# Performance work log

Measured on AMD Instinct MI355X. Metric: run time of the kernel, lower is better.

Reference implementation:

```python
import jax, jax.numpy as jnp
from jax import lax
import numpy as np

B, T = 32, 64
E, H, V = 512, 512, 10000


def setup_inputs() -> dict:
    key = jax.random.key(0)
    ks = jax.random.split(key, 9)
    s = 0.02
    return {
        "features": jax.random.normal(ks[0], (B, E), dtype=jnp.float32),
        "captions": jax.random.randint(ks[1], (B, T), 0, V, dtype=jnp.int64),
        "forward_approach": 0,
        "embed_table": jax.random.normal(ks[2], (V, E), dtype=jnp.float32) * s,
        "W_ih": jax.random.normal(ks[3], (4 * H, E), dtype=jnp.float32) * s,
        "W_hh": jax.random.normal(ks[4], (4 * H, H), dtype=jnp.float32) * s,
        "b_ih": jax.random.normal(ks[5], (4 * H,), dtype=jnp.float32) * s,
        "b_hh": jax.random.normal(ks[6], (4 * H,), dtype=jnp.float32) * s,
        "fc_W": jax.random.normal(ks[7], (V, H), dtype=jnp.float32) * s,
        "fc_b": jax.random.normal(ks[8], (V,), dtype=jnp.float32) * s,
    }


def reference(features, captions, forward_approach, embed_table,
              W_ih, W_hh, b_ih, b_hh, fc_W, fc_b):
    # features: [B, E]; captions: [B, T] int
    batch = features.shape[0]
    seq_len = captions.shape[1]
    hidden = W_hh.shape[1]

    # Input at step 0 is `features`; at step t>0 it is embed(captions[:, t-1]).
    emb = embed_table[captions[:, : seq_len - 1]]            # [B, T-1, E]
    xs = jnp.concatenate([features[None], jnp.transpose(emb, (1, 0, 2))],
                         axis=0)                              # [T, B, E]

    def step(carry, x):
        h, c = carry
        # PyTorch LSTMCell gate order: i, f, g, o
        gates = x @ W_ih.T + b_ih + h @ W_hh.T + b_hh         # [B, 4H]
        i, f, g, o = jnp.split(gates, 4, axis=-1)
        i = jax.nn.sigmoid(i)
        f = jax.nn.sigmoid(f)
        g = jnp.tanh(g)
        o = jax.nn.sigmoid(o)
        c = f * c + i * g
        h = o * jnp.tanh(c)
        return (h, c), h

    h0 = jnp.zeros((batch, hidden), dtype=features.dtype)
    c0 = jnp.zeros((batch, hidden), dtype=features.dtype)
    _, hs = lax.scan(step, (h0, c0), xs)                      # [T, B, H]

    logits = jnp.einsum('tbh,vh->tbv', hs, fc_W) + fc_b       # [T, B, V]
    return jnp.transpose(logits, (1, 0, 2))                   # [B, T, V]
```

## Files before the change

### kernel.cpp

```cpp
#include <hip/hip_runtime.h>
#include <hip/hip_bf16.h>

#define B_ 32
#define T_ 64
#define E_ 512
#define H_ 512
#define V_ 10000
#define G4 2048

#define NLSTM 64
#define NFC   157
#define NTOT  (NLSTM + NFC)

using bf16x8 = __attribute__((ext_vector_type(8))) short;
using f32x4  = __attribute__((ext_vector_type(4))) float;

__device__ inline f32x4 mfma16(bf16x8 a, bf16x8 b, f32x4 c) {
  return __builtin_amdgcn_mfma_f32_16x16x32_bf16(a, b, c, 0, 0, 0);
}

__device__ inline short f2bf(float x) {
  unsigned u = __builtin_bit_cast(unsigned, x);
  u = (u + 0x7fffu + ((u >> 16) & 1u)) >> 16;
  return (short)u;
}

__device__ inline float fsigm(float x) {
  return __builtin_amdgcn_rcpf(1.f + __builtin_amdgcn_exp2f(-1.442695040888963f * x));
}
__device__ inline float ftanh(float x) {
  return 1.f - 2.f * __builtin_amdgcn_rcpf(1.f + __builtin_amdgcn_exp2f(2.885390081777927f * x));
}

__device__ inline bf16x8 lds_ld16B(const short* base, int row, int col) {
  int byte = (row << 10) + (col << 1);
  byte ^= (row & 7) << 4;
  return *(const bf16x8*)((const char*)base + byte);
}

__device__ inline bf16x8 cast8(const float* src) {
  float4 f0 = *(const float4*)src;
  float4 f1 = *(const float4*)(src + 4);
  bf16x8 v;
  v[0] = f2bf(f0.x); v[1] = f2bf(f0.y); v[2] = f2bf(f0.z); v[3] = f2bf(f0.w);
  v[4] = f2bf(f1.x); v[5] = f2bf(f1.y); v[6] = f2bf(f1.z); v[7] = f2bf(f1.w);
  return v;
}


__global__ void prep_kernel(const float* __restrict__ b_ih, const float* __restrict__ b_hh,
                            const float* __restrict__ features, const int* __restrict__ captions,
                            const float* __restrict__ embed,
                            float* __restrict__ bsum, short* __restrict__ xs) {
  int i = blockIdx.x * blockDim.x + threadIdx.x;
  int stride = gridDim.x * blockDim.x;
  const int NA = G4;
  const int NB = NA + T_ * B_ * E_;
  for (; i < NB; i += stride) {
    if (i < NA) {
      bsum[i] = b_ih[i] + b_hh[i];
    } else {
      int j = i - NA;
      int t = j / (B_ * E_);
      int r = j - t * (B_ * E_);
      int b = r >> 9;
      int e = r & 511;
      float v;
      if (t == 0) v = features[b * E_ + e];
      else        v = embed[captions[b * T_ + (t - 1)] * E_ + e];
      xs[j] = f2bf(v);
    }
  }
}


__global__ __launch_bounds__(256) void fused_kernel(const float* __restrict__ WhhF,
                                                    const float* __restrict__ WihF,
                                                    const float* __restrict__ bsum,
                                                    const short* __restrict__ xs,
                                                    short* __restrict__ hs,
                                                    int* __restrict__ flags,
                                                    const float* __restrict__ fcWF,
                                                    const float* __restrict__ fcbias,
                                                    float* __restrict__ out) {
  __shared__ short Wlds[2 * 64 * 512];
  __shared__ int tready;
  const int tid = threadIdx.x;
  int* const cnt = flags + 256;

  if (blockIdx.x < NLSTM) {
    const int blk  = blockIdx.x;
    const int bg   = blk >> 5;
    const int slot = blk & 31;
    const int hc0  = slot * 16;
    int* const gflags = flags + bg * 32;

    for (int i = tid * 8; i < 2 * 64 * 512; i += 256 * 8) {
      int region = i >> 15;
      int local  = i & 32767;
      int gc = local >> 9;
      int k  = local & 511;
      int g  = gc >> 4, c = gc & 15;
      const float* src = (region ? WihF : WhhF) + (size_t)(g * 512 + hc0 + c) * 512 + k;
      bf16x8 v = cast8(src);
      int byte = ((local * 2) ^ ((gc & 7) << 4)) + (region << 16);
      *(bf16x8*)((char*)Wlds + byte) = v;
    }
    __syncthreads();
    if (tid >= 64) return;

    const short* WB = Wlds + 64 * 512;
    const int lane = tid;
    const int lr  = lane & 15;
    const int ko  = (lane >> 4) << 3;
    const int cr  = (lane >> 4) << 2;
    const int cc  = lane & 15;
    const int bat = bg * 16 + cc;
    const int brow = bg * 16 + lr;

    float4 bb0 = *(const float4*)&bsum[0 * 512 + hc0 + cr];
    float4 bb1 = *(const float4*)&bsum[1 * 512 + hc0 + cr];
    float4 bb2 = *(const float4*)&bsum[2 * 512 + hc0 + cr];
    float4 bb3 = *(const float4*)&bsum[3 * 512 + hc0 + cr];

    float cst[4] = {0.f, 0.f, 0.f, 0.f};

    for (int t = 0; t < T_; ++t) {
      f32x4 a0 = {}, a1 = {}, a2 = {}, a3 = {};
      {
        const short* Ax = xs + ((size_t)t * B_ + brow) * 512 + ko;
#pragma unroll
        for (int kk = 0; kk < 512; kk += 32) {
          bf16x8 xb = *(const bf16x8*)(Ax + kk);
          bf16x8 w0 = lds_ld16B(WB,      lr, kk + ko);
          bf16x8 w1 = lds_ld16B(WB, 16 + lr, kk + ko);
          bf16x8 w2 = lds_ld16B(WB, 32 + lr, kk + ko);
          bf16x8 w3 = lds_ld16B(WB, 48 + lr, kk + ko);
          a0 = mfma16(w0, xb, a0);
          a1 = mfma16(w1, xb, a1);
          a2 = mfma16(w2, xb, a2);
          a3 = mfma16(w3, xb, a3);
        }
      }
      if (t > 0) {
        const int* fp = gflags + (lane & 31);
        for (;;) {
          int fl = __hip_atomic_load(fp, __ATOMIC_RELAXED, __HIP_MEMORY_SCOPE_AGENT);
          if (__all(fl >= t)) break;
        }
        asm volatile("" ::: "memory");
        const short* Ap = hs + (size_t)(t - 1) * (B_ * H_) + brow * 512 + ko;
#pragma unroll
        for (int kk = 0; kk < 512; kk += 32) {
          bf16x8 hb = *(const bf16x8*)(Ap + kk);
          bf16x8 w0 = lds_ld16B(Wlds,      lr, kk + ko);
          bf16x8 w1 = lds_ld16B(Wlds, 16 + lr, kk + ko);
          bf16x8 w2 = lds_ld16B(Wlds, 32 + lr, kk + ko);
          bf16x8 w3 = lds_ld16B(Wlds, 48 + lr, kk + ko);
          a0 = mfma16(w0, hb, a0);
          a1 = mfma16(w1, hb, a1);
          a2 = mfma16(w2, hb, a2);
          a3 = mfma16(w3, hb, a3);
        }
      }
      unsigned long long hpack = 0;
#pragma unroll
      for (int j = 0; j < 4; ++j) {
        float iv = fsigm(a0[j] + ((const float*)&bb0)[j]);
        float fv = fsigm(a1[j] + ((const float*)&bb1)[j]);
        float gv = ftanh(a2[j] + ((const float*)&bb2)[j]);
        float ov = fsigm(a3[j] + ((const float*)&bb3)[j]);
        float cv = fv * cst[j] + iv * gv;
        cst[j] = cv;
        float hv = ov * ftanh(cv);
        hpack |= (unsigned long long)(unsigned short)f2bf(hv) << (16 * j);
      }
      __hip_atomic_store(
          (unsigned long long*)(hs + (size_t)t * (B_ * H_) + bat * 512 + hc0 + cr),
          hpack, __ATOMIC_RELAXED, __HIP_MEMORY_SCOPE_AGENT);
      asm volatile("s_waitcnt vmcnt(0)" ::: "memory");
      if (lane == 0) {
        if (t < T_ - 1)
          __hip_atomic_store(gflags + slot, t + 1, __ATOMIC_RELAXED,
                             __HIP_MEMORY_SCOPE_AGENT);
        __hip_atomic_fetch_add(cnt + t, 1, __ATOMIC_RELAXED,
                               __HIP_MEMORY_SCOPE_AGENT);
      }
    }
  } else {
    const int fblk = blockIdx.x - NLSTM;
    const int n0   = fblk * 64;
    const int lane = tid & 63;
    const int wv   = tid >> 6;
    const int lr   = lane & 15;
    const int ko   = (lane >> 4) << 3;

    if (tid == 0)
      __hip_atomic_store(&tready, 0, __ATOMIC_RELAXED, __HIP_MEMORY_SCOPE_WORKGROUP);

    for (int i = tid * 8; i < 64 * 512; i += 256 * 8) {
      int gc = i >> 9;
      int k  = i & 511;
      int nr = n0 + gc; if (nr >= V_) nr = V_ - 1;
      bf16x8 v = cast8(fcWF + (size_t)nr * 512 + k);
      int byte = (i * 2) ^ ((gc & 7) << 4);
      *(bf16x8*)((char*)Wlds + byte) = v;
    }
    __syncthreads();

    const int cr = (lane >> 4) * 4, cc = lane & 15;
    const int colw = n0 + wv * 16 + cc;
    const bool wok = colw < V_;
    const float bias = wok ? fcbias[colw] : 0.f;

    for (int t = 0; t < T_; ++t) {
      if (wv == 0) {
        for (;;) {
          int c = __hip_atomic_load(cnt + t, __ATOMIC_RELAXED,
                                    __HIP_MEMORY_SCOPE_AGENT);
          if (c >= NLSTM) break;
          __builtin_amdgcn_s_sleep(32);
        }
        __hip_atomic_store(&tready, t + 1, __ATOMIC_RELAXED,
                           __HIP_MEMORY_SCOPE_WORKGROUP);
      } else {
        while (__hip_atomic_load(&tready, __ATOMIC_RELAXED,
                                 __HIP_MEMORY_SCOPE_WORKGROUP) < t + 1)
          __builtin_amdgcn_s_sleep(2);
      }
      asm volatile("" ::: "memory");
      const short* Ap = hs + (size_t)t * (B_ * H_) + lr * 512 + ko;
      f32x4 acc0 = {}, acc1 = {};
#pragma unroll
      for (int k = 0; k < 512; k += 32) {
        bf16x8 a0 = *(const bf16x8*)(Ap + k);
        bf16x8 a1 = *(const bf16x8*)(Ap + 16 * 512 + k);
        bf16x8 b  = lds_ld16B(Wlds, wv * 16 + lr, k + ko);
        acc0 = mfma16(a0, b, acc0);
        acc1 = mfma16(a1, b, acc1);
      }
      if (wok) {
#pragma unroll
        for (int j = 0; j < 4; ++j) {
          out[(size_t)(cr + j) * (T_ * V_) + t * V_ + colw]      = acc0[j] + bias;
          out[(size_t)(16 + cr + j) * (T_ * V_) + t * V_ + colw] = acc1[j] + bias;
        }
      }
    }
  }
}


extern "C" void kernel_launch(void* const* d_in, const int* in_sizes, int n_in,
                              void* d_out, int out_size, void* d_ws, size_t ws_size,
                              hipStream_t stream) {
  const float* features = (const float*)d_in[0];
  const int*   captions = (const int*)d_in[1];
  const float* embed    = (const float*)d_in[3];
  const float* W_ih     = (const float*)d_in[4];
  const float* W_hh     = (const float*)d_in[5];
  const float* b_ih     = (const float*)d_in[6];
  const float* b_hh     = (const float*)d_in[7];
  const float* fc_W     = (const float*)d_in[8];
  const float* fc_b     = (const float*)d_in[9];
  float* out = (float*)d_out;

  char* ws = (char*)d_ws;
  size_t off = 0;
  auto alloc = [&](size_t bytes) -> void* {
    off = (off + 255) & ~(size_t)255;
    void* p = ws + off;
    off += bytes;
    return p;
  };
  int*      flags = (int*)  alloc(4096);
  float*    bsum  = (float*)alloc((size_t)G4 * 4);
  short*    xs    = (short*)alloc((size_t)T_ * B_ * E_ * 2);
  short*    hs    = (short*)alloc((size_t)T_ * B_ * H_ * 2);

  (void)hipMemsetAsync(flags, 0, 4096, stream);
  prep_kernel<<<1024, 256, 0, stream>>>(b_ih, b_hh, features, captions, embed,
                                        bsum, xs);
  fused_kernel<<<NTOT, 256, 0, stream>>>(W_hh, W_ih, bsum, xs, hs, flags,
                                         fc_W, fc_b, out);
}
```

Before: 277.4 us.

## Map LSTM groups to single XCDs and sync recurrence via XCD-local flags

```diff
diff --git a/kernel.cpp b/kernel.cpp
--- a/kernel.cpp
+++ b/kernel.cpp
@@ -8,9 +8,8 @@
 #define V_ 10000
 #define G4 2048
 
-#define NLSTM 64
 #define NFC   157
-#define NTOT  (NLSTM + NFC)
+#define NTOT  256
 
 using bf16x8 = __attribute__((ext_vector_type(8))) short;
 using f32x4  = __attribute__((ext_vector_type(4))) float;
@@ -79,116 +78,201 @@
                                                     const float* __restrict__ bsum,
                                                     const short* __restrict__ xs,
                                                     short* __restrict__ hs,
-                                                    int* __restrict__ flags,
+                                                    int* __restrict__ comm,
                                                     const float* __restrict__ fcWF,
                                                     const float* __restrict__ fcbias,
                                                     float* __restrict__ out) {
   __shared__ short Wlds[2 * 64 * 512];
   __shared__ int tready;
+  __shared__ int hmail;
   const int tid = threadIdx.x;
-  int* const cnt = flags + 256;
-
-  if (blockIdx.x < NLSTM) {
-    const int blk  = blockIdx.x;
-    const int bg   = blk >> 5;
-    const int slot = blk & 31;
+  const int m8  = blockIdx.x & 7;
+  int* const cnt = comm + 256;
+
+  if (m8 < 2) {
+    const int g    = m8;
+    const int slot = blockIdx.x >> 3;
     const int hc0  = slot * 16;
-    int* const gflags = flags + bg * 32;
-
+    int* const gflags = comm + g * 32;
+    int* const lflags = comm + 64 + g * 32;
+    int* const pub    = comm + 128 + g * 32;
+
+    unsigned xcd;
+    asm volatile("s_getreg_b32 %0, hwreg(HW_REG_XCC_ID)" : "=s"(xcd));
+    if (tid == 0) {
+      tready = 0;
+      hmail  = 0;
+      __hip_atomic_store(pub + slot, (int)(xcd & 7) + 1, __ATOMIC_RELAXED,
+                         __HIP_MEMORY_SCOPE_AGENT);
+    }
     for (int i = tid * 8; i < 2 * 64 * 512; i += 256 * 8) {
       int region = i >> 15;
       int local  = i & 32767;
       int gc = local >> 9;
       int k  = local & 511;
-      int g  = gc >> 4, c = gc & 15;
-      const float* src = (region ? WihF : WhhF) + (size_t)(g * 512 + hc0 + c) * 512 + k;
+      int gg = gc >> 4, c = gc & 15;
+      const float* src = (region ? WihF : WhhF) + (size_t)(gg * 512 + hc0 + c) * 512 + k;
       bf16x8 v = cast8(src);
       int byte = ((local * 2) ^ ((gc & 7) << 4)) + (region << 16);
       *(bf16x8*)((char*)Wlds + byte) = v;
     }
     __syncthreads();
-    if (tid >= 64) return;
-
-    const short* WB = Wlds + 64 * 512;
-    const int lane = tid;
+
+    const int wv   = tid >> 6;
+    const int lane = tid & 63;
+    if (wv >= 2) return;
+
     const int lr  = lane & 15;
     const int ko  = (lane >> 4) << 3;
     const int cr  = (lane >> 4) << 2;
     const int cc  = lane & 15;
-    const int bat = bg * 16 + cc;
-    const int brow = bg * 16 + lr;
-
-    float4 bb0 = *(const float4*)&bsum[0 * 512 + hc0 + cr];
-    float4 bb1 = *(const float4*)&bsum[1 * 512 + hc0 + cr];
-    float4 bb2 = *(const float4*)&bsum[2 * 512 + hc0 + cr];
-    float4 bb3 = *(const float4*)&bsum[3 * 512 + hc0 + cr];
-
-    float cst[4] = {0.f, 0.f, 0.f, 0.f};
-
-    for (int t = 0; t < T_; ++t) {
-      f32x4 a0 = {}, a1 = {}, a2 = {}, a3 = {};
-      {
-        const short* Ax = xs + ((size_t)t * B_ + brow) * 512 + ko;
-#pragma unroll
-        for (int kk = 0; kk < 512; kk += 32) {
-          bf16x8 xb = *(const bf16x8*)(Ax + kk);
-          bf16x8 w0 = lds_ld16B(WB,      lr, kk + ko);
-          bf16x8 w1 = lds_ld16B(WB, 16 + lr, kk + ko);
-          bf16x8 w2 = lds_ld16B(WB, 32 + lr, kk + ko);
-          bf16x8 w3 = lds_ld16B(WB, 48 + lr, kk + ko);
-          a0 = mfma16(w0, xb, a0);
-          a1 = mfma16(w1, xb, a1);
-          a2 = mfma16(w2, xb, a2);
-          a3 = mfma16(w3, xb, a3);
-        }
-      }
-      if (t > 0) {
-        const int* fp = gflags + (lane & 31);
-        for (;;) {
-          int fl = __hip_atomic_load(fp, __ATOMIC_RELAXED, __HIP_MEMORY_SCOPE_AGENT);
-          if (__all(fl >= t)) break;
-        }
+    const int bat = g * 16 + cc;
+    const int brow = g * 16 + lr;
+
+    if (wv == 0) {
+      const int* pp = pub + (lane & 31);
+      int pv;
+      for (;;) {
+        pv = __hip_atomic_load(pp, __ATOMIC_RELAXED, __HIP_MEMORY_SCOPE_AGENT);
+        if (__all(pv != 0)) break;
+        __builtin_amdgcn_s_sleep(1);
+      }
+      const bool use_local = __all(pv == __shfl(pv, 0));
+      if (lane == 0)
+        __hip_atomic_store(&tready, use_local ? 2 : 1, __ATOMIC_RELAXED,
+                           __HIP_MEMORY_SCOPE_WORKGROUP);
+
+      const short* WB = Wlds + 64 * 512;
+      float4 bb0 = *(const float4*)&bsum[0 * 512 + hc0 + cr];
+      float4 bb1 = *(const float4*)&bsum[1 * 512 + hc0 + cr];
+      float4 bb2 = *(const float4*)&bsum[2 * 512 + hc0 + cr];
+      float4 bb3 = *(const float4*)&bsum[3 * 512 + hc0 + cr];
+      float cst[4] = {0.f, 0.f, 0.f, 0.f};
+
+      for (int t = 0; t < T_; ++t) {
+        f32x4 a0 = {}, a1 = {}, a2 = {}, a3 = {};
+        {
+          const short* Ax = xs + ((size_t)t * B_ + brow) * 512 + ko;
+#pragma unroll
+          for (int kk = 0; kk < 512; kk += 32) {
+            bf16x8 xb = *(const bf16x8*)(Ax + kk);
+            bf16x8 w0 = lds_ld16B(WB,      lr, kk + ko);
+            bf16x8 w1 = lds_ld16B(WB, 16 + lr, kk + ko);
+            bf16x8 w2 = lds_ld16B(WB, 32 + lr, kk + ko);
+            bf16x8 w3 = lds_ld16B(WB, 48 + lr, kk + ko);
+            a0 = mfma16(w0, xb, a0);
+            a1 = mfma16(w1, xb, a1);
+            a2 = mfma16(w2, xb, a2);
+            a3 = mfma16(w3, xb, a3);
+          }
+        }
+        if (t > 0) {
+          if (use_local) {
+            const int* lp = lflags + (lane & 31);
+            bool got = false;
+            for (int it = 0; it < 64 && !got; ++it) {
+              int fl;
+              asm volatile("global_load_dword %0, %1, off sc0\n\t"
+                           "s_waitcnt vmcnt(0)"
+                           : "=v"(fl) : "v"(lp) : "memory");
+              got = __all(fl >= t);
+            }
+            if (!got) {
+              const int* fp = gflags + (lane & 31);
+              for (;;) {
+                int fl = __hip_atomic_load(fp, __ATOMIC_RELAXED, __HIP_MEMORY_SCOPE_AGENT);
+                if (__all(fl >= t)) break;
+                __builtin_amdgcn_s_sleep(1);
+              }
+            }
+          } else {
+            const int* fp = gflags + (lane & 31);
+            for (;;) {
+              int fl = __hip_atomic_load(fp, __ATOMIC_RELAXED, __HIP_MEMORY_SCOPE_AGENT);
+              if (__all(fl >= t)) break;
+            }
+          }
+          asm volatile("" ::: "memory");
+          const short* Ap = hs + (size_t)(t - 1) * (B_ * H_) + brow * 512 + ko;
+#pragma unroll
+          for (int kk = 0; kk < 512; kk += 32) {
+            bf16x8 hb = *(const bf16x8*)(Ap + kk);
+            bf16x8 w0 = lds_ld16B(Wlds,      lr, kk + ko);
+            bf16x8 w1 = lds_ld16B(Wlds, 16 + lr, kk + ko);
+            bf16x8 w2 = lds_ld16B(Wlds, 32 + lr, kk + ko);
+            bf16x8 w3 = lds_ld16B(Wlds, 48 + lr, kk + ko);
+            a0 = mfma16(w0, hb, a0);
+            a1 = mfma16(w1, hb, a1);
+            a2 = mfma16(w2, hb, a2);
+            a3 = mfma16(w3, hb, a3);
+          }
+        }
+        unsigned long long hpack = 0;
+#pragma unroll
+        for (int j = 0; j < 4; ++j) {
+          float iv = fsigm(a0[j] + ((const float*)&bb0)[j]);
+          float fv = fsigm(a1[j] + ((const float*)&bb1)[j]);
+          float gv = ftanh(a2[j] + ((const float*)&bb2)[j]);
+          float ov = fsigm(a3[j] + ((const float*)&bb3)[j]);
+          float cv = fv * cst[j] + iv * gv;
+          cst[j] = cv;
+          float hv = ov * ftanh(cv);
+          hpack |= (unsigned long long)(unsigned short)f2bf(hv) << (16 * j);
+        }
+        unsigned long long* hp8 =
+            (unsigned long long*)(hs + (size_t)t * (B_ * H_) + bat * 512 + hc0 + cr);
+        if (use_local) {
+          *hp8 = hpack;
+          asm volatile("s_waitcnt vmcnt(0)" ::: "memory");
+          if (lane == 0) {
+            if (t < T_ - 1) {
+              int* lfp = lflags + slot;
+              int  fv2 = t + 1;
+              asm volatile("global_store_dword %0, %1, off" :: "v"(lfp), "v"(fv2) : "memory");
+            }
+            __hip_atomic_store(&hmail, t + 1, __ATOMIC_RELAXED,
+                               __HIP_MEMORY_SCOPE_WORKGROUP);
+          }
+        } else {
+          __hip_atomic_store(hp8, hpack, __ATOMIC_RELAXED, __HIP_MEMORY_SCOPE_AGENT);
+          asm volatile("s_waitcnt vmcnt(0)" ::: "memory");
+          if (lane == 0) {
+            if (t < T_ - 1)
+              __hip_atomic_store(gflags + slot, t + 1, __ATOMIC_RELAXED,
+                                 __HIP_MEMORY_SCOPE_AGENT);
+            __hip_atomic_fetch_add(cnt + t, 1, __ATOMIC_RELAXED,
+                                   __HIP_MEMORY_SCOPE_AGENT);
+          }
+        }
+      }
+    } else {
+      int mode;
+      do {
+        mode = __hip_atomic_load(&tready, __ATOMIC_RELAXED, __HIP_MEMORY_SCOPE_WORKGROUP);
+        if (mode == 0) __builtin_amdgcn_s_sleep(1);
+      } while (mode == 0);
+      if (mode != 2) return;
+      for (int t = 0; t < T_; ++t) {
+        while (__hip_atomic_load(&hmail, __ATOMIC_RELAXED,
+                                 __HIP_MEMORY_SCOPE_WORKGROUP) < t + 1)
+          __builtin_amdgcn_s_sleep(1);
         asm volatile("" ::: "memory");
-        const short* Ap = hs + (size_t)(t - 1) * (B_ * H_) + brow * 512 + ko;
-#pragma unroll
-        for (int kk = 0; kk < 512; kk += 32) {
-          bf16x8 hb = *(const bf16x8*)(Ap + kk);
-          bf16x8 w0 = lds_ld16B(Wlds,      lr, kk + ko);
-          bf16x8 w1 = lds_ld16B(Wlds, 16 + lr, kk + ko);
-          bf16x8 w2 = lds_ld16B(Wlds, 32 + lr, kk + ko);
-          bf16x8 w3 = lds_ld16B(Wlds, 48 + lr, kk + ko);
-          a0 = mfma16(w0, hb, a0);
-          a1 = mfma16(w1, hb, a1);
-          a2 = mfma16(w2, hb, a2);
-          a3 = mfma16(w3, hb, a3);
-        }
-      }
-      unsigned long long hpack = 0;
-#pragma unroll
-      for (int j = 0; j < 4; ++j) {
-        float iv = fsigm(a0[j] + ((const float*)&bb0)[j]);
-        float fv = fsigm(a1[j] + ((const float*)&bb1)[j]);
-        float gv = ftanh(a2[j] + ((const float*)&bb2)[j]);
-        float ov = fsigm(a3[j] + ((const float*)&bb3)[j]);
-        float cv = fv * cst[j] + iv * gv;
-        cst[j] = cv;
-        float hv = ov * ftanh(cv);
-        hpack |= (unsigned long long)(unsigned short)f2bf(hv) << (16 * j);
-      }
-      __hip_atomic_store(
-          (unsigned long long*)(hs + (size_t)t * (B_ * H_) + bat * 512 + hc0 + cr),
-          hpack, __ATOMIC_RELAXED, __HIP_MEMORY_SCOPE_AGENT);
-      asm volatile("s_waitcnt vmcnt(0)" ::: "memory");
-      if (lane == 0) {
-        if (t < T_ - 1)
+        unsigned long long* hp8 =
+            (unsigned long long*)(hs + (size_t)t * (B_ * H_) + bat * 512 + hc0 + cr);
+        unsigned long long v = *hp8;
+        __hip_atomic_store(hp8, v, __ATOMIC_RELAXED, __HIP_MEMORY_SCOPE_AGENT);
+        asm volatile("s_waitcnt vmcnt(0)" ::: "memory");
+        if (lane == 0) {
           __hip_atomic_store(gflags + slot, t + 1, __ATOMIC_RELAXED,
                              __HIP_MEMORY_SCOPE_AGENT);
-        __hip_atomic_fetch_add(cnt + t, 1, __ATOMIC_RELAXED,
-                               __HIP_MEMORY_SCOPE_AGENT);
+          __hip_atomic_fetch_add(cnt + t, 1, __ATOMIC_RELAXED,
+                                 __HIP_MEMORY_SCOPE_AGENT);
+        }
       }
     }
   } else {
-    const int fblk = blockIdx.x - NLSTM;
+    const int fblk = (blockIdx.x >> 3) * 6 + (m8 - 2);
+    if (fblk >= NFC) return;
     const int n0   = fblk * 64;
     const int lane = tid & 63;
     const int wv   = tid >> 6;
@@ -218,7 +302,7 @@
         for (;;) {
           int c = __hip_atomic_load(cnt + t, __ATOMIC_RELAXED,
                                     __HIP_MEMORY_SCOPE_AGENT);
-          if (c >= NLSTM) break;
+          if (c >= 64) break;
           __builtin_amdgcn_s_sleep(32);
         }
         __hip_atomic_store(&tready, t + 1, __ATOMIC_RELAXED,
@@ -273,14 +357,14 @@
     off += bytes;
     return p;
   };
-  int*      flags = (int*)  alloc(4096);
-  float*    bsum  = (float*)alloc((size_t)G4 * 4);
-  short*    xs    = (short*)alloc((size_t)T_ * B_ * E_ * 2);
-  short*    hs    = (short*)alloc((size_t)T_ * B_ * H_ * 2);
-
-  (void)hipMemsetAsync(flags, 0, 4096, stream);
+  int*      comm = (int*)  alloc(4096);
+  float*    bsum = (float*)alloc((size_t)G4 * 4);
+  short*    xs   = (short*)alloc((size_t)T_ * B_ * E_ * 2);
+  short*    hs   = (short*)alloc((size_t)T_ * B_ * H_ * 2);
+
+  (void)hipMemsetAsync(comm, 0, 4096, stream);
   prep_kernel<<<1024, 256, 0, stream>>>(b_ih, b_hh, features, captions, embed,
                                         bsum, xs);
-  fused_kernel<<<NTOT, 256, 0, stream>>>(W_hh, W_ih, bsum, xs, hs, flags,
+  fused_kernel<<<NTOT, 256, 0, stream>>>(W_hh, W_ih, bsum, xs, hs, comm,
                                          fc_W, fc_b, out);
 }
```

Measured after the change: 288.5 us. 1.04x slower.

## Fuse embedding gather and bias sum into the LSTM kernel, drop prep launch

Applied to the files above, without the earlier changes.

```diff
diff --git a/kernel.cpp b/kernel.cpp
--- a/kernel.cpp
+++ b/kernel.cpp
@@ -48,42 +48,20 @@
 }
 
 
-__global__ void prep_kernel(const float* __restrict__ b_ih, const float* __restrict__ b_hh,
-                            const float* __restrict__ features, const int* __restrict__ captions,
-                            const float* __restrict__ embed,
-                            float* __restrict__ bsum, short* __restrict__ xs) {
-  int i = blockIdx.x * blockDim.x + threadIdx.x;
-  int stride = gridDim.x * blockDim.x;
-  const int NA = G4;
-  const int NB = NA + T_ * B_ * E_;
-  for (; i < NB; i += stride) {
-    if (i < NA) {
-      bsum[i] = b_ih[i] + b_hh[i];
-    } else {
-      int j = i - NA;
-      int t = j / (B_ * E_);
-      int r = j - t * (B_ * E_);
-      int b = r >> 9;
-      int e = r & 511;
-      float v;
-      if (t == 0) v = features[b * E_ + e];
-      else        v = embed[captions[b * T_ + (t - 1)] * E_ + e];
-      xs[j] = f2bf(v);
-    }
-  }
-}
-
-
 __global__ __launch_bounds__(256) void fused_kernel(const float* __restrict__ WhhF,
                                                     const float* __restrict__ WihF,
-                                                    const float* __restrict__ bsum,
-                                                    const short* __restrict__ xs,
+                                                    const float* __restrict__ b_ih,
+                                                    const float* __restrict__ b_hh,
+                                                    const float* __restrict__ features,
+                                                    const int* __restrict__ captions,
+                                                    const float* __restrict__ embed,
                                                     short* __restrict__ hs,
                                                     int* __restrict__ flags,
                                                     const float* __restrict__ fcWF,
                                                     const float* __restrict__ fcbias,
                                                     float* __restrict__ out) {
   __shared__ short Wlds[2 * 64 * 512];
+  __shared__ int cap_lds[16][64];
   __shared__ int tready;
   const int tid = threadIdx.x;
   int* const cnt = flags + 256;
@@ -106,6 +84,11 @@
       int byte = ((local * 2) ^ ((gc & 7) << 4)) + (region << 16);
       *(bf16x8*)((char*)Wlds + byte) = v;
     }
+    for (int i = tid; i < 16 * 63; i += 256) {
+      int b = i / 63;
+      int t = i - b * 63 + 1;
+      cap_lds[b][t] = captions[(bg * 16 + b) * T_ + (t - 1)];
+    }
     __syncthreads();
     if (tid >= 64) return;
 
@@ -118,20 +101,33 @@
     const int bat = bg * 16 + cc;
     const int brow = bg * 16 + lr;
 
-    float4 bb0 = *(const float4*)&bsum[0 * 512 + hc0 + cr];
-    float4 bb1 = *(const float4*)&bsum[1 * 512 + hc0 + cr];
-    float4 bb2 = *(const float4*)&bsum[2 * 512 + hc0 + cr];
-    float4 bb3 = *(const float4*)&bsum[3 * 512 + hc0 + cr];
+    float4 bb0, bb1, bb2, bb3;
+    {
+      float4 i0 = *(const float4*)&b_ih[0 * 512 + hc0 + cr];
+      float4 h0 = *(const float4*)&b_hh[0 * 512 + hc0 + cr];
+      float4 i1 = *(const float4*)&b_ih[1 * 512 + hc0 + cr];
+      float4 h1 = *(const float4*)&b_hh[1 * 512 + hc0 + cr];
+      float4 i2 = *(const float4*)&b_ih[2 * 512 + hc0 + cr];
+      float4 h2 = *(const float4*)&b_hh[2 * 512 + hc0 + cr];
+      float4 i3 = *(const float4*)&b_ih[3 * 512 + hc0 + cr];
+      float4 h3 = *(const float4*)&b_hh[3 * 512 + hc0 + cr];
+      bb0 = make_float4(i0.x + h0.x, i0.y + h0.y, i0.z + h0.z, i0.w + h0.w);
+      bb1 = make_float4(i1.x + h1.x, i1.y + h1.y, i1.z + h1.z, i1.w + h1.w);
+      bb2 = make_float4(i2.x + h2.x, i2.y + h2.y, i2.z + h2.z, i2.w + h2.w);
+      bb3 = make_float4(i3.x + h3.x, i3.y + h3.y, i3.z + h3.z, i3.w + h3.w);
+    }
 
     float cst[4] = {0.f, 0.f, 0.f, 0.f};
 
     for (int t = 0; t < T_; ++t) {
       f32x4 a0 = {}, a1 = {}, a2 = {}, a3 = {};
       {
-        const short* Ax = xs + ((size_t)t * B_ + brow) * 512 + ko;
+        const float* xrow = (t == 0)
+            ? features + (size_t)brow * 512
+            : embed + (size_t)cap_lds[lr][t] * 512;
 #pragma unroll
         for (int kk = 0; kk < 512; kk += 32) {
-          bf16x8 xb = *(const bf16x8*)(Ax + kk);
+          bf16x8 xb = cast8(xrow + kk + ko);
           bf16x8 w0 = lds_ld16B(WB,      lr, kk + ko);
           bf16x8 w1 = lds_ld16B(WB, 16 + lr, kk + ko);
           bf16x8 w2 = lds_ld16B(WB, 32 + lr, kk + ko);
@@ -273,14 +269,11 @@
     off += bytes;
     return p;
   };
-  int*      flags = (int*)  alloc(4096);
-  float*    bsum  = (float*)alloc((size_t)G4 * 4);
-  short*    xs    = (short*)alloc((size_t)T_ * B_ * E_ * 2);
-  short*    hs    = (short*)alloc((size_t)T_ * B_ * H_ * 2);
+  int*   flags = (int*)  alloc(4096);
+  short* hs    = (short*)alloc((size_t)T_ * B_ * H_ * 2);
 
   (void)hipMemsetAsync(flags, 0, 4096, stream);
-  prep_kernel<<<1024, 256, 0, stream>>>(b_ih, b_hh, features, captions, embed,
-                                        bsum, xs);
-  fused_kernel<<<NTOT, 256, 0, stream>>>(W_hh, W_ih, bsum, xs, hs, flags,
-                                         fc_W, fc_b, out);
-}
+  fused_kernel<<<NTOT, 256, 0, stream>>>(W_hh, W_ih, b_ih, b_hh,
+                                         features, captions, embed,
+                                         hs, flags, fc_W, fc_b, out);
+}
```

After: 538.7 us. 1.94x slower.
